# Performance work log

Hardware: AMD Instinct MI355X
Metric: run time of the kernel (lower is better)

The kernel has to match this reference:

```python
import jax, jax.numpy as jnp
import numpy as np

B = 2048
VOCABS = [100000, 50000, 10, 3, 100, 50, 1000, 24, 5]  # user,item,age,gender,city,category,brand,hour,device
E = 16
EMB_DIMS = [E, E, E // 2, E // 4, E // 2, E // 2, E // 2, E // 4, E // 4]
NUM_FEATURES = sum(VOCABS) + 1  # +1 for the price column
DEEP_IN = sum(EMB_DIMS) + 1  # 77
HIDDEN = [256, 128, 64]


def setup_inputs() -> dict:
    key = jax.random.key(0)
    ks = iter(jax.random.split(key, 40))
    inp = {}
    names = ['user_id', 'item_id', 'age', 'gender', 'city', 'category', 'brand', 'hour', 'device']
    for name, v in zip(names, VOCABS):
        inp[name] = jax.random.randint(next(ks), (B, 1), 0, v, dtype=jnp.int32).astype(jnp.int64)
    inp['price'] = jax.random.uniform(next(ks), (B, 1), dtype=jnp.float32) * 100.0
    # embedding tables
    tab_names = ['emb_user', 'emb_item', 'emb_age', 'emb_gender', 'emb_city', 'emb_category', 'emb_brand', 'emb_hour', 'emb_device']
    for name, v, d in zip(tab_names, VOCABS, EMB_DIMS):
        inp[name] = jax.random.normal(next(ks), (v, d), dtype=jnp.float32) * 0.05
    # dense (1st-order) weights
    inp['w_dense'] = jax.random.normal(next(ks), (NUM_FEATURES,), dtype=jnp.float32) * 0.01
    inp['b_dense'] = jnp.zeros((), dtype=jnp.float32)
    # FM 2nd-order factors
    inp['fm_v'] = jax.random.normal(next(ks), (NUM_FEATURES, E), dtype=jnp.float32) * 0.01
    # deep MLP
    dims = [DEEP_IN] + HIDDEN
    for i in range(len(HIDDEN)):
        inp[f'W{i+1}'] = jax.random.normal(next(ks), (dims[i], dims[i + 1]), dtype=jnp.float32) * (1.0 / np.sqrt(dims[i]))
        inp[f'b{i+1}'] = jnp.zeros((dims[i + 1],), dtype=jnp.float32)
    inp['Wo'] = jax.random.normal(next(ks), (HIDDEN[-1], 1), dtype=jnp.float32) * (1.0 / np.sqrt(HIDDEN[-1]))
    inp['bo'] = jnp.zeros((1,), dtype=jnp.float32)
    return inp


def reference(user_id, item_id, age, gender, city, category, brand, price, hour, device,
              emb_user, emb_item, emb_age, emb_gender, emb_city, emb_category, emb_brand,
              emb_hour, emb_device, w_dense, b_dense, fm_v, W1, b1, W2, b2, W3, b3, Wo, bo):
    b = user_id.shape[0]
    rows = jnp.arange(b)
    ids = [user_id, item_id, age, gender, city, category, brand, hour, device]
    # one-hot style feature vector: (b, NUM_FEATURES)
    feat = jnp.zeros((b, NUM_FEATURES), dtype=price.dtype)
    off = 0
    for idx, v in zip(ids, VOCABS):
        feat = feat.at[rows, off + idx[:, 0]].set(1.0)
        off += v
    feat = feat.at[:, NUM_FEATURES - 1].set(price[:, 0] / 1000.0)

    # 1st-order linear part
    logit_dense = feat @ w_dense + b_dense  # (b,)

    # FM 2nd-order: 0.5 * sum_k [ (x@V)^2 - x^2 @ V^2 ]
    square_of_sum = jnp.square(feat @ fm_v)            # (b, E)
    sum_of_square = jnp.square(feat) @ jnp.square(fm_v)  # (b, E)
    logit_fm = 0.5 * jnp.sum(square_of_sum - sum_of_square, axis=1)  # (b,)

    # deep part: embedding lookups + MLP (dropout inactive / eval mode)
    tables = [emb_user, emb_item, emb_age, emb_gender, emb_city, emb_category, emb_brand, emb_hour, emb_device]
    embs = [t[i[:, 0]] for t, i in zip(tables, ids)]
    deep_in = jnp.concatenate(embs + [price], axis=1)  # (b, 77)
    h = jax.nn.relu(deep_in @ W1 + b1)
    h = jax.nn.relu(h @ W2 + b2)
    h = jax.nn.relu(h @ W3 + b3)
    logit_deep = (h @ Wo + bo)[:, 0]

    return logit_dense + logit_fm + logit_deep
```

## Files before the change

kernel.cpp:

```cpp
#include <hip/hip_runtime.h>


#define RPB 4
#define BATCH 2048
#define NF 151193

#define OFF0 0
#define OFF1 100000
#define OFF2 150000
#define OFF3 150010
#define OFF4 150013
#define OFF5 150113
#define OFF6 150163
#define OFF7 151163
#define OFF8 151187

typedef float f4 __attribute__((ext_vector_type(4)));

__device__ inline f4 relu4(f4 v) {
    f4 r;
    r.x = fmaxf(v.x, 0.0f); r.y = fmaxf(v.y, 0.0f);
    r.z = fmaxf(v.z, 0.0f); r.w = fmaxf(v.w, 0.0f);
    return r;
}

__global__ __launch_bounds__(256, 2) void deepfm_fused(
    const int* __restrict__ f_user, const int* __restrict__ f_item,
    const int* __restrict__ f_age, const int* __restrict__ f_gender,
    const int* __restrict__ f_city, const int* __restrict__ f_cat,
    const int* __restrict__ f_brand, const int* __restrict__ f_hour,
    const int* __restrict__ f_dev, const float* __restrict__ price,
    const float* __restrict__ e_user, const float* __restrict__ e_item,
    const float* __restrict__ e_age, const float* __restrict__ e_gender,
    const float* __restrict__ e_city, const float* __restrict__ e_cat,
    const float* __restrict__ e_brand, const float* __restrict__ e_hour,
    const float* __restrict__ e_dev,
    const float* __restrict__ w_dense, const float* __restrict__ b_dense,
    const float* __restrict__ fm_v,
    const float* __restrict__ W1, const float* __restrict__ b1,
    const float* __restrict__ W2, const float* __restrict__ b2,
    const float* __restrict__ W3, const float* __restrict__ b3,
    const float* __restrict__ Wo, const float* __restrict__ bo,
    float* __restrict__ out)
{
    __shared__ __align__(16) float x[RPB][80];
    __shared__ __align__(16) float h1s[RPB][256];
    __shared__ __align__(16) float h2s[RPB][128];
    __shared__ __align__(16) float h3s[RPB][64];
    __shared__ __align__(16) float pred[4096];
    __shared__ float row_extra[RPB];
    __shared__ float spx[RPB];
    __shared__ int   sid[RPB][9];

    const int tid  = threadIdx.x;
    const int base = blockIdx.x * RPB;

    if (tid < RPB) {
        const int gr = base + tid;
        sid[tid][0] = f_user[gr];
        sid[tid][1] = f_item[gr];
        sid[tid][2] = f_age[gr];
        sid[tid][3] = f_gender[gr];
        sid[tid][4] = f_city[gr];
        sid[tid][5] = f_cat[gr];
        sid[tid][6] = f_brand[gr];
        sid[tid][7] = f_hour[gr];
        sid[tid][8] = f_dev[gr];
        spx[tid]    = price[gr];
    }
    __syncthreads();

    if (tid < 128) {
        const int r = tid >> 5, l = tid & 31;
        if (l < 16) x[r][ 0 + l] = e_user  [sid[r][0] * 16 + l];
        if (l < 16) x[r][16 + l] = e_item  [sid[r][1] * 16 + l];
        if (l <  8) x[r][32 + l] = e_age   [sid[r][2] *  8 + l];
        if (l <  4) x[r][40 + l] = e_gender[sid[r][3] *  4 + l];
        if (l <  8) x[r][44 + l] = e_city  [sid[r][4] *  8 + l];
        if (l <  8) x[r][52 + l] = e_cat   [sid[r][5] *  8 + l];
        if (l <  8) x[r][60 + l] = e_brand [sid[r][6] *  8 + l];
        if (l <  4) x[r][68 + l] = e_hour  [sid[r][7] *  4 + l];
        if (l <  4) x[r][72 + l] = e_dev   [sid[r][8] *  4 + l];
        if (l == 0) x[r][76]     = spx[r];
        if (l == 1) { x[r][77] = 0.0f; }
        if (l == 2) { x[r][78] = 0.0f; }
        if (l == 3) { x[r][79] = 0.0f; }
    } else if (tid < 192) {
        const int r = (tid >> 4) & 3, k = tid & 15;
        const float px = spx[r] * (1.0f / 1000.0f);
        float v, s, ssq;
        v = fm_v[(NF - 1) * 16 + k];
        s = px * v; ssq = s * s;
        v = fm_v[(OFF0 + sid[r][0]) * 16 + k]; s += v; ssq += v * v;
        v = fm_v[(OFF1 + sid[r][1]) * 16 + k]; s += v; ssq += v * v;
        v = fm_v[(OFF2 + sid[r][2]) * 16 + k]; s += v; ssq += v * v;
        v = fm_v[(OFF3 + sid[r][3]) * 16 + k]; s += v; ssq += v * v;
        v = fm_v[(OFF4 + sid[r][4]) * 16 + k]; s += v; ssq += v * v;
        v = fm_v[(OFF5 + sid[r][5]) * 16 + k]; s += v; ssq += v * v;
        v = fm_v[(OFF6 + sid[r][6]) * 16 + k]; s += v; ssq += v * v;
        v = fm_v[(OFF7 + sid[r][7]) * 16 + k]; s += v; ssq += v * v;
        v = fm_v[(OFF8 + sid[r][8]) * 16 + k]; s += v; ssq += v * v;
        float q = 0.5f * (s * s - ssq);
        if (k == 0) {
            float d = b_dense[0] + px * w_dense[NF - 1];
            d += w_dense[OFF0 + sid[r][0]];
            d += w_dense[OFF1 + sid[r][1]];
            d += w_dense[OFF2 + sid[r][2]];
            d += w_dense[OFF3 + sid[r][3]];
            d += w_dense[OFF4 + sid[r][4]];
            d += w_dense[OFF5 + sid[r][5]];
            d += w_dense[OFF6 + sid[r][6]];
            d += w_dense[OFF7 + sid[r][7]];
            d += w_dense[OFF8 + sid[r][8]];
            q += d;
        }
        q += __shfl_xor(q, 8);
        q += __shfl_xor(q, 4);
        q += __shfl_xor(q, 2);
        q += __shfl_xor(q, 1);
        if (k == 0) row_extra[r] = q;
    }
    __syncthreads();

    {
        const int kg = tid >> 6, ct = tid & 63;
        const f4* W1v = (const f4*)W1;
        const f4* xv  = (const f4*)x;
        f4 acc0 = 0, acc1 = 0, acc2 = 0, acc3 = 0;
        const int i0 = 20 * kg;
        const int nch = (kg == 3) ? 4 : 5;
        for (int c = 0; c < nch; ++c) {
            const int i = i0 + 4 * c, q = i >> 2;
            f4 xa0 = xv[ 0 + q];
            f4 xa1 = xv[20 + q];
            f4 xa2 = xv[40 + q];
            f4 xa3 = xv[60 + q];
            f4 w0 = W1v[(i + 0) * 64 + ct];
            f4 w1 = W1v[(i + 1) * 64 + ct];
            f4 w2 = W1v[(i + 2) * 64 + ct];
            f4 w3 = W1v[(i + 3) * 64 + ct];
            acc0 += xa0.x * w0 + xa0.y * w1 + xa0.z * w2 + xa0.w * w3;
            acc1 += xa1.x * w0 + xa1.y * w1 + xa1.z * w2 + xa1.w * w3;
            acc2 += xa2.x * w0 + xa2.y * w1 + xa2.z * w2 + xa2.w * w3;
            acc3 += xa3.x * w0 + xa3.y * w1 + xa3.z * w2 + xa3.w * w3;
        }
        if (kg == 3) {
            f4 w = W1v[76 * 64 + ct];
            acc0 += x[0][76] * w;
            acc1 += x[1][76] * w;
            acc2 += x[2][76] * w;
            acc3 += x[3][76] * w;
        }
        f4* pv = (f4*)pred;
        pv[(kg * 4 + 0) * 64 + ct] = acc0;
        pv[(kg * 4 + 1) * 64 + ct] = acc1;
        pv[(kg * 4 + 2) * 64 + ct] = acc2;
        pv[(kg * 4 + 3) * 64 + ct] = acc3;
    }
    __syncthreads();
    {
        const int r = tid >> 6, c4 = tid & 63;
        const f4* pv = (const f4*)pred;
        f4 s = pv[(0 + r) * 64 + c4] + pv[(4 + r) * 64 + c4]
             + pv[(8 + r) * 64 + c4] + pv[(12 + r) * 64 + c4];
        s += ((const f4*)b1)[c4];
        ((f4*)h1s)[r * 64 + c4] = relu4(s);
    }
    __syncthreads();

    {
        const int kg = tid >> 5, ct = tid & 31;
        const f4* W2v = (const f4*)W2;
        const f4* hv  = (const f4*)h1s;
        f4 acc0 = 0, acc1 = 0, acc2 = 0, acc3 = 0;
        const int i0 = 32 * kg;
        #pragma unroll
        for (int c = 0; c < 8; ++c) {
            const int i = i0 + 4 * c, q = i >> 2;
            f4 xa0 = hv[  0 + q];
            f4 xa1 = hv[ 64 + q];
            f4 xa2 = hv[128 + q];
            f4 xa3 = hv[192 + q];
            f4 w0 = W2v[(i + 0) * 32 + ct];
            f4 w1 = W2v[(i + 1) * 32 + ct];
            f4 w2 = W2v[(i + 2) * 32 + ct];
            f4 w3 = W2v[(i + 3) * 32 + ct];
            acc0 += xa0.x * w0 + xa0.y * w1 + xa0.z * w2 + xa0.w * w3;
            acc1 += xa1.x * w0 + xa1.y * w1 + xa1.z * w2 + xa1.w * w3;
            acc2 += xa2.x * w0 + xa2.y * w1 + xa2.z * w2 + xa2.w * w3;
            acc3 += xa3.x * w0 + xa3.y * w1 + xa3.z * w2 + xa3.w * w3;
        }
        f4* pv = (f4*)pred;
        pv[(kg * 4 + 0) * 32 + ct] = acc0;
        pv[(kg * 4 + 1) * 32 + ct] = acc1;
        pv[(kg * 4 + 2) * 32 + ct] = acc2;
        pv[(kg * 4 + 3) * 32 + ct] = acc3;
    }
    __syncthreads();
    if (tid < 128) {
        const int r = tid >> 5, c4 = tid & 31;
        const f4* pv = (const f4*)pred;
        f4 s = 0;
        #pragma unroll
        for (int kg = 0; kg < 8; ++kg) s += pv[(kg * 4 + r) * 32 + c4];
        s += ((const f4*)b2)[c4];
        ((f4*)h2s)[r * 32 + c4] = relu4(s);
    }
    __syncthreads();

    {
        const int kg = tid >> 4, ct = tid & 15;
        const f4* W3v = (const f4*)W3;
        const f4* hv  = (const f4*)h2s;
        f4 acc0 = 0, acc1 = 0, acc2 = 0, acc3 = 0;
        const int i0 = 8 * kg;
        #pragma unroll
        for (int c = 0; c < 2; ++c) {
            const int i = i0 + 4 * c, q = i >> 2;
            f4 xa0 = hv[ 0 + q];
            f4 xa1 = hv[32 + q];
            f4 xa2 = hv[64 + q];
            f4 xa3 = hv[96 + q];
            f4 w0 = W3v[(i + 0) * 16 + ct];
            f4 w1 = W3v[(i + 1) * 16 + ct];
            f4 w2 = W3v[(i + 2) * 16 + ct];
            f4 w3 = W3v[(i + 3) * 16 + ct];
            acc0 += xa0.x * w0 + xa0.y * w1 + xa0.z * w2 + xa0.w * w3;
            acc1 += xa1.x * w0 + xa1.y * w1 + xa1.z * w2 + xa1.w * w3;
            acc2 += xa2.x * w0 + xa2.y * w1 + xa2.z * w2 + xa2.w * w3;
            acc3 += xa3.x * w0 + xa3.y * w1 + xa3.z * w2 + xa3.w * w3;
        }
        f4* pv = (f4*)pred;
        pv[(kg * 4 + 0) * 16 + ct] = acc0;
        pv[(kg * 4 + 1) * 16 + ct] = acc1;
        pv[(kg * 4 + 2) * 16 + ct] = acc2;
        pv[(kg * 4 + 3) * 16 + ct] = acc3;
    }
    __syncthreads();
    if (tid < 64) {
        const int r = tid >> 4, c4 = tid & 15;
        const f4* pv = (const f4*)pred;
        f4 s = 0;
        #pragma unroll
        for (int kg = 0; kg < 16; ++kg) s += pv[(kg * 4 + r) * 16 + c4];
        s += ((const f4*)b3)[c4];
        ((f4*)h3s)[r * 16 + c4] = relu4(s);
    }
    __syncthreads();

    if (tid < 128) {
        const int r = tid >> 5, l = tid & 31;
        float a = h3s[r][l] * Wo[l] + h3s[r][l + 32] * Wo[l + 32];
        a += __shfl_xor(a, 16);
        a += __shfl_xor(a, 8);
        a += __shfl_xor(a, 4);
        a += __shfl_xor(a, 2);
        a += __shfl_xor(a, 1);
        if (l == 0) out[base + r] = a + bo[0] + row_extra[r];
    }
}

extern "C" void kernel_launch(void* const* d_in, const int* in_sizes, int n_in,
                              void* d_out, int out_size, void* d_ws, size_t ws_size,
                              hipStream_t stream) {
    const int*   f_user   = (const int*)  d_in[0];
    const int*   f_item   = (const int*)  d_in[1];
    const int*   f_age    = (const int*)  d_in[2];
    const int*   f_gender = (const int*)  d_in[3];
    const int*   f_city   = (const int*)  d_in[4];
    const int*   f_cat    = (const int*)  d_in[5];
    const int*   f_brand  = (const int*)  d_in[6];
    const int*   f_hour   = (const int*)  d_in[7];
    const int*   f_dev    = (const int*)  d_in[8];
    const float* price    = (const float*)d_in[9];
    const float* e_user   = (const float*)d_in[10];
    const float* e_item   = (const float*)d_in[11];
    const float* e_age    = (const float*)d_in[12];
    const float* e_gender = (const float*)d_in[13];
    const float* e_city   = (const float*)d_in[14];
    const float* e_cat    = (const float*)d_in[15];
    const float* e_brand  = (const float*)d_in[16];
    const float* e_hour   = (const float*)d_in[17];
    const float* e_dev    = (const float*)d_in[18];
    const float* w_dense  = (const float*)d_in[19];
    const float* b_dense  = (const float*)d_in[20];
    const float* fm_v     = (const float*)d_in[21];
    const float* W1       = (const float*)d_in[22];
    const float* b1       = (const float*)d_in[23];
    const float* W2       = (const float*)d_in[24];
    const float* b2       = (const float*)d_in[25];
    const float* W3       = (const float*)d_in[26];
    const float* b3       = (const float*)d_in[27];
    const float* Wo       = (const float*)d_in[28];
    const float* bo       = (const float*)d_in[29];
    float* out = (float*)d_out;

    dim3 grid(BATCH / RPB);
    dim3 block(256);
    deepfm_fused<<<grid, block, 0, stream>>>(
        f_user, f_item, f_age, f_gender, f_city, f_cat, f_brand, f_hour, f_dev,
        price, e_user, e_item, e_age, e_gender, e_city, e_cat, e_brand, e_hour,
        e_dev, w_dense, b_dense, fm_v, W1, b1, W2, b2, W3, b3, Wo, bo, out);
}
```

Measured before the change: 132.1 us.

## Prefetch MLP weights into registers ahead of each layer and drop index staging

Loads W1 into registers at kernel start, then prefetches W2 and W3 into registers during the previous layer's compute, so weight loads overlap with earlier stages. Also removes the shared-memory staging of ids and price, so each thread reads them directly. The final ReLU and output projection are fused into the layer-3 reduction, which saves one barrier. The cost is much higher register pressure (about 60 f4 values), which may lower occupancy or cause spills.

```diff
diff --git a/kernel.cpp b/kernel.cpp
--- a/kernel.cpp
+++ b/kernel.cpp
@@ -46,72 +46,76 @@
     __shared__ __align__(16) float x[RPB][80];
     __shared__ __align__(16) float h1s[RPB][256];
     __shared__ __align__(16) float h2s[RPB][128];
-    __shared__ __align__(16) float h3s[RPB][64];
     __shared__ __align__(16) float pred[4096];
     __shared__ float row_extra[RPB];
-    __shared__ float spx[RPB];
-    __shared__ int   sid[RPB][9];
 
     const int tid  = threadIdx.x;
     const int base = blockIdx.x * RPB;
 
-    if (tid < RPB) {
-        const int gr = base + tid;
-        sid[tid][0] = f_user[gr];
-        sid[tid][1] = f_item[gr];
-        sid[tid][2] = f_age[gr];
-        sid[tid][3] = f_gender[gr];
-        sid[tid][4] = f_city[gr];
-        sid[tid][5] = f_cat[gr];
-        sid[tid][6] = f_brand[gr];
-        sid[tid][7] = f_hour[gr];
-        sid[tid][8] = f_dev[gr];
-        spx[tid]    = price[gr];
-    }
-    __syncthreads();
+    const f4* W1v = (const f4*)W1;
+    const int kg1 = tid >> 6, ct1 = tid & 63;
+    f4 w1r[20];
+    {
+        const int i0 = 20 * kg1;
+        #pragma unroll
+        for (int d = 0; d < 20; ++d) {
+            const int i = i0 + d;
+            w1r[d] = (i < 77) ? W1v[i * 64 + ct1] : (f4)0.0f;
+        }
+    }
+    const f4 b1v  = ((const f4*)b1)[tid & 63];
+    const f4 b2v  = ((const f4*)b2)[tid & 31];
+    const f4 b3v  = ((const f4*)b3)[tid & 15];
+    const f4 wo_r = ((const f4*)Wo)[tid & 15];
+    const float bo_s = bo[0];
 
     if (tid < 128) {
         const int r = tid >> 5, l = tid & 31;
-        if (l < 16) x[r][ 0 + l] = e_user  [sid[r][0] * 16 + l];
-        if (l < 16) x[r][16 + l] = e_item  [sid[r][1] * 16 + l];
-        if (l <  8) x[r][32 + l] = e_age   [sid[r][2] *  8 + l];
-        if (l <  4) x[r][40 + l] = e_gender[sid[r][3] *  4 + l];
-        if (l <  8) x[r][44 + l] = e_city  [sid[r][4] *  8 + l];
-        if (l <  8) x[r][52 + l] = e_cat   [sid[r][5] *  8 + l];
-        if (l <  8) x[r][60 + l] = e_brand [sid[r][6] *  8 + l];
-        if (l <  4) x[r][68 + l] = e_hour  [sid[r][7] *  4 + l];
-        if (l <  4) x[r][72 + l] = e_dev   [sid[r][8] *  4 + l];
-        if (l == 0) x[r][76]     = spx[r];
-        if (l == 1) { x[r][77] = 0.0f; }
-        if (l == 2) { x[r][78] = 0.0f; }
-        if (l == 3) { x[r][79] = 0.0f; }
+        const int gr = base + r;
+        if (l < 16) x[r][ 0 + l] = e_user  [f_user[gr]   * 16 + l];
+        if (l < 16) x[r][16 + l] = e_item  [f_item[gr]   * 16 + l];
+        if (l <  8) x[r][32 + l] = e_age   [f_age[gr]    *  8 + l];
+        if (l <  4) x[r][40 + l] = e_gender[f_gender[gr] *  4 + l];
+        if (l <  8) x[r][44 + l] = e_city  [f_city[gr]   *  8 + l];
+        if (l <  8) x[r][52 + l] = e_cat   [f_cat[gr]    *  8 + l];
+        if (l <  8) x[r][60 + l] = e_brand [f_brand[gr]  *  8 + l];
+        if (l <  4) x[r][68 + l] = e_hour  [f_hour[gr]   *  4 + l];
+        if (l <  4) x[r][72 + l] = e_dev   [f_dev[gr]    *  4 + l];
+        if (l == 0) x[r][76]     = price[gr];
+        if (l == 1) x[r][77] = 0.0f;
+        if (l == 2) x[r][78] = 0.0f;
+        if (l == 3) x[r][79] = 0.0f;
     } else if (tid < 192) {
         const int r = (tid >> 4) & 3, k = tid & 15;
-        const float px = spx[r] * (1.0f / 1000.0f);
+        const int gr = base + r;
+        const int i0 = f_user[gr], i1 = f_item[gr], i2 = f_age[gr];
+        const int i3 = f_gender[gr], i4 = f_city[gr], i5 = f_cat[gr];
+        const int i6 = f_brand[gr], i7 = f_hour[gr], i8 = f_dev[gr];
+        const float px = price[gr] * (1.0f / 1000.0f);
         float v, s, ssq;
         v = fm_v[(NF - 1) * 16 + k];
         s = px * v; ssq = s * s;
-        v = fm_v[(OFF0 + sid[r][0]) * 16 + k]; s += v; ssq += v * v;
-        v = fm_v[(OFF1 + sid[r][1]) * 16 + k]; s += v; ssq += v * v;
-        v = fm_v[(OFF2 + sid[r][2]) * 16 + k]; s += v; ssq += v * v;
-        v = fm_v[(OFF3 + sid[r][3]) * 16 + k]; s += v; ssq += v * v;
-        v = fm_v[(OFF4 + sid[r][4]) * 16 + k]; s += v; ssq += v * v;
-        v = fm_v[(OFF5 + sid[r][5]) * 16 + k]; s += v; ssq += v * v;
-        v = fm_v[(OFF6 + sid[r][6]) * 16 + k]; s += v; ssq += v * v;
-        v = fm_v[(OFF7 + sid[r][7]) * 16 + k]; s += v; ssq += v * v;
-        v = fm_v[(OFF8 + sid[r][8]) * 16 + k]; s += v; ssq += v * v;
+        v = fm_v[(OFF0 + i0) * 16 + k]; s += v; ssq += v * v;
+        v = fm_v[(OFF1 + i1) * 16 + k]; s += v; ssq += v * v;
+        v = fm_v[(OFF2 + i2) * 16 + k]; s += v; ssq += v * v;
+        v = fm_v[(OFF3 + i3) * 16 + k]; s += v; ssq += v * v;
+        v = fm_v[(OFF4 + i4) * 16 + k]; s += v; ssq += v * v;
+        v = fm_v[(OFF5 + i5) * 16 + k]; s += v; ssq += v * v;
+        v = fm_v[(OFF6 + i6) * 16 + k]; s += v; ssq += v * v;
+        v = fm_v[(OFF7 + i7) * 16 + k]; s += v; ssq += v * v;
+        v = fm_v[(OFF8 + i8) * 16 + k]; s += v; ssq += v * v;
         float q = 0.5f * (s * s - ssq);
         if (k == 0) {
             float d = b_dense[0] + px * w_dense[NF - 1];
-            d += w_dense[OFF0 + sid[r][0]];
-            d += w_dense[OFF1 + sid[r][1]];
-            d += w_dense[OFF2 + sid[r][2]];
-            d += w_dense[OFF3 + sid[r][3]];
-            d += w_dense[OFF4 + sid[r][4]];
-            d += w_dense[OFF5 + sid[r][5]];
-            d += w_dense[OFF6 + sid[r][6]];
-            d += w_dense[OFF7 + sid[r][7]];
-            d += w_dense[OFF8 + sid[r][8]];
+            d += w_dense[OFF0 + i0];
+            d += w_dense[OFF1 + i1];
+            d += w_dense[OFF2 + i2];
+            d += w_dense[OFF3 + i3];
+            d += w_dense[OFF4 + i4];
+            d += w_dense[OFF5 + i5];
+            d += w_dense[OFF6 + i6];
+            d += w_dense[OFF7 + i7];
+            d += w_dense[OFF8 + i8];
             q += d;
         }
         q += __shfl_xor(q, 8);
@@ -122,75 +126,70 @@
     }
     __syncthreads();
 
-    {
-        const int kg = tid >> 6, ct = tid & 63;
-        const f4* W1v = (const f4*)W1;
-        const f4* xv  = (const f4*)x;
+    const f4* hv1 = (const f4*)h1s;
+    const f4* hv2 = (const f4*)h2s;
+    f4* pv = (f4*)pred;
+    f4 w2r[32];
+    {
+        const f4* xv = (const f4*)x;
         f4 acc0 = 0, acc1 = 0, acc2 = 0, acc3 = 0;
-        const int i0 = 20 * kg;
-        const int nch = (kg == 3) ? 4 : 5;
-        for (int c = 0; c < nch; ++c) {
-            const int i = i0 + 4 * c, q = i >> 2;
+        #pragma unroll
+        for (int c = 0; c < 5; ++c) {
+            const int q = 5 * kg1 + c;
             f4 xa0 = xv[ 0 + q];
             f4 xa1 = xv[20 + q];
             f4 xa2 = xv[40 + q];
             f4 xa3 = xv[60 + q];
-            f4 w0 = W1v[(i + 0) * 64 + ct];
-            f4 w1 = W1v[(i + 1) * 64 + ct];
-            f4 w2 = W1v[(i + 2) * 64 + ct];
-            f4 w3 = W1v[(i + 3) * 64 + ct];
-            acc0 += xa0.x * w0 + xa0.y * w1 + xa0.z * w2 + xa0.w * w3;
-            acc1 += xa1.x * w0 + xa1.y * w1 + xa1.z * w2 + xa1.w * w3;
-            acc2 += xa2.x * w0 + xa2.y * w1 + xa2.z * w2 + xa2.w * w3;
-            acc3 += xa3.x * w0 + xa3.y * w1 + xa3.z * w2 + xa3.w * w3;
-        }
-        if (kg == 3) {
-            f4 w = W1v[76 * 64 + ct];
-            acc0 += x[0][76] * w;
-            acc1 += x[1][76] * w;
-            acc2 += x[2][76] * w;
-            acc3 += x[3][76] * w;
-        }
-        f4* pv = (f4*)pred;
-        pv[(kg * 4 + 0) * 64 + ct] = acc0;
-        pv[(kg * 4 + 1) * 64 + ct] = acc1;
-        pv[(kg * 4 + 2) * 64 + ct] = acc2;
-        pv[(kg * 4 + 3) * 64 + ct] = acc3;
+            acc0 += xa0.x * w1r[4*c] + xa0.y * w1r[4*c+1] + xa0.z * w1r[4*c+2] + xa0.w * w1r[4*c+3];
+            acc1 += xa1.x * w1r[4*c] + xa1.y * w1r[4*c+1] + xa1.z * w1r[4*c+2] + xa1.w * w1r[4*c+3];
+            acc2 += xa2.x * w1r[4*c] + xa2.y * w1r[4*c+1] + xa2.z * w1r[4*c+2] + xa2.w * w1r[4*c+3];
+            acc3 += xa3.x * w1r[4*c] + xa3.y * w1r[4*c+1] + xa3.z * w1r[4*c+2] + xa3.w * w1r[4*c+3];
+        }
+        {
+            const int kg = tid >> 5, ct = tid & 31;
+            const f4* W2v = (const f4*)W2;
+            const int i0 = 32 * kg;
+            #pragma unroll
+            for (int d = 0; d < 32; ++d) w2r[d] = W2v[(i0 + d) * 32 + ct];
+        }
+        pv[(kg1 * 4 + 0) * 64 + ct1] = acc0;
+        pv[(kg1 * 4 + 1) * 64 + ct1] = acc1;
+        pv[(kg1 * 4 + 2) * 64 + ct1] = acc2;
+        pv[(kg1 * 4 + 3) * 64 + ct1] = acc3;
     }
     __syncthreads();
     {
         const int r = tid >> 6, c4 = tid & 63;
-        const f4* pv = (const f4*)pred;
         f4 s = pv[(0 + r) * 64 + c4] + pv[(4 + r) * 64 + c4]
              + pv[(8 + r) * 64 + c4] + pv[(12 + r) * 64 + c4];
-        s += ((const f4*)b1)[c4];
+        s += b1v;
         ((f4*)h1s)[r * 64 + c4] = relu4(s);
     }
     __syncthreads();
 
+    f4 w3r[8];
     {
         const int kg = tid >> 5, ct = tid & 31;
-        const f4* W2v = (const f4*)W2;
-        const f4* hv  = (const f4*)h1s;
         f4 acc0 = 0, acc1 = 0, acc2 = 0, acc3 = 0;
-        const int i0 = 32 * kg;
         #pragma unroll
         for (int c = 0; c < 8; ++c) {
-            const int i = i0 + 4 * c, q = i >> 2;
-            f4 xa0 = hv[  0 + q];
-            f4 xa1 = hv[ 64 + q];
-            f4 xa2 = hv[128 + q];
-            f4 xa3 = hv[192 + q];
-            f4 w0 = W2v[(i + 0) * 32 + ct];
-            f4 w1 = W2v[(i + 1) * 32 + ct];
-            f4 w2 = W2v[(i + 2) * 32 + ct];
-            f4 w3 = W2v[(i + 3) * 32 + ct];
-            acc0 += xa0.x * w0 + xa0.y * w1 + xa0.z * w2 + xa0.w * w3;
-            acc1 += xa1.x * w0 + xa1.y * w1 + xa1.z * w2 + xa1.w * w3;
-            acc2 += xa2.x * w0 + xa2.y * w1 + xa2.z * w2 + xa2.w * w3;
-            acc3 += xa3.x * w0 + xa3.y * w1 + xa3.z * w2 + xa3.w * w3;
-        }
-        f4* pv = (f4*)pred;
+            const int q = 8 * kg + c;
+            f4 xa0 = hv1[  0 + q];
+            f4 xa1 = hv1[ 64 + q];
+            f4 xa2 = hv1[128 + q];
+            f4 xa3 = hv1[192 + q];
+            acc0 += xa0.x * w2r[4*c] + xa0.y * w2r[4*c+1] + xa0.z * w2r[4*c+2] + xa0.w * w2r[4*c+3];
+            acc1 += xa1.x * w2r[4*c] + xa1.y * w2r[4*c+1] + xa1.z * w2r[4*c+2] + xa1.w * w2r[4*c+3];
+            acc2 += xa2.x * w2r[4*c] + xa2.y * w2r[4*c+1] + xa2.z * w2r[4*c+2] + xa2.w * w2r[4*c+3];
+            acc3 += xa3.x * w2r[4*c] + xa3.y * w2r[4*c+1] + xa3.z * w2r[4*c+2] + xa3.w * w2r[4*c+3];
+        }
+        {
+            const int kg3 = tid >> 4, ct3 = tid & 15;
+            const f4* W3v = (const f4*)W3;
+            const int i0 = 8 * kg3;
+            #pragma unroll
+            for (int d = 0; d < 8; ++d) w3r[d] = W3v[(i0 + d) * 16 + ct3];
+        }
         pv[(kg * 4 + 0) * 32 + ct] = acc0;
         pv[(kg * 4 + 1) * 32 + ct] = acc1;
         pv[(kg * 4 + 2) * 32 + ct] = acc2;
@@ -199,64 +198,49 @@
     __syncthreads();
     if (tid < 128) {
         const int r = tid >> 5, c4 = tid & 31;
-        const f4* pv = (const f4*)pred;
         f4 s = 0;
         #pragma unroll
         for (int kg = 0; kg < 8; ++kg) s += pv[(kg * 4 + r) * 32 + c4];
-        s += ((const f4*)b2)[c4];
+        s += b2v;
         ((f4*)h2s)[r * 32 + c4] = relu4(s);
     }
     __syncthreads();
 
     {
         const int kg = tid >> 4, ct = tid & 15;
-        const f4* W3v = (const f4*)W3;
-        const f4* hv  = (const f4*)h2s;
         f4 acc0 = 0, acc1 = 0, acc2 = 0, acc3 = 0;
-        const int i0 = 8 * kg;
         #pragma unroll
         for (int c = 0; c < 2; ++c) {
-            const int i = i0 + 4 * c, q = i >> 2;
-            f4 xa0 = hv[ 0 + q];
-            f4 xa1 = hv[32 + q];
-            f4 xa2 = hv[64 + q];
-            f4 xa3 = hv[96 + q];
-            f4 w0 = W3v[(i + 0) * 16 + ct];
-            f4 w1 = W3v[(i + 1) * 16 + ct];
-            f4 w2 = W3v[(i + 2) * 16 + ct];
-            f4 w3 = W3v[(i + 3) * 16 + ct];
-            acc0 += xa0.x * w0 + xa0.y * w1 + xa0.z * w2 + xa0.w * w3;
-            acc1 += xa1.x * w0 + xa1.y * w1 + xa1.z * w2 + xa1.w * w3;
-            acc2 += xa2.x * w0 + xa2.y * w1 + xa2.z * w2 + xa2.w * w3;
-            acc3 += xa3.x * w0 + xa3.y * w1 + xa3.z * w2 + xa3.w * w3;
-        }
-        f4* pv = (f4*)pred;
+            const int q = 2 * kg + c;
+            f4 xa0 = hv2[ 0 + q];
+            f4 xa1 = hv2[32 + q];
+            f4 xa2 = hv2[64 + q];
+            f4 xa3 = hv2[96 + q];
+            acc0 += xa0.x * w3r[4*c] + xa0.y * w3r[4*c+1] + xa0.z * w3r[4*c+2] + xa0.w * w3r[4*c+3];
+            acc1 += xa1.x * w3r[4*c] + xa1.y * w3r[4*c+1] + xa1.z * w3r[4*c+2] + xa1.w * w3r[4*c+3];
+            acc2 += xa2.x * w3r[4*c] + xa2.y * w3r[4*c+1] + xa2.z * w3r[4*c+2] + xa2.w * w3r[4*c+3];
+            acc3 += xa3.x * w3r[4*c] + xa3.y * w3r[4*c+1] + xa3.z * w3r[4*c+2] + xa3.w * w3r[4*c+3];
+        }
         pv[(kg * 4 + 0) * 16 + ct] = acc0;
         pv[(kg * 4 + 1) * 16 + ct] = acc1;
         pv[(kg * 4 + 2) * 16 + ct] = acc2;
         pv[(kg * 4 + 3) * 16 + ct] = acc3;
     }
     __syncthreads();
+
     if (tid < 64) {
         const int r = tid >> 4, c4 = tid & 15;
-        const f4* pv = (const f4*)pred;
         f4 s = 0;
         #pragma unroll
         for (int kg = 0; kg < 16; ++kg) s += pv[(kg * 4 + r) * 16 + c4];
-        s += ((const f4*)b3)[c4];
-        ((f4*)h3s)[r * 16 + c4] = relu4(s);
-    }
-    __syncthreads();
-
-    if (tid < 128) {
-        const int r = tid >> 5, l = tid & 31;
-        float a = h3s[r][l] * Wo[l] + h3s[r][l + 32] * Wo[l + 32];
-        a += __shfl_xor(a, 16);
-        a += __shfl_xor(a, 8);
-        a += __shfl_xor(a, 4);
-        a += __shfl_xor(a, 2);
-        a += __shfl_xor(a, 1);
-        if (l == 0) out[base + r] = a + bo[0] + row_extra[r];
+        s += b3v;
+        f4 h = relu4(s);
+        float t = h.x * wo_r.x + h.y * wo_r.y + h.z * wo_r.z + h.w * wo_r.w;
+        t += __shfl_xor(t, 8);
+        t += __shfl_xor(t, 4);
+        t += __shfl_xor(t, 2);
+        t += __shfl_xor(t, 1);
+        if (c4 == 0) out[base + r] = t + bo_s + row_extra[r];
     }
 }
 
```

After: 133.2 us. Within noise of the previous version (+0.8%).
